# Kernel optimization log

Measured on AMD Instinct MI355X. Metric: run time of the kernel, lower is better.

## Reference

```python
import jax, jax.numpy as jnp
import numpy as np

LOAD = 0.001 / np.sqrt(2.0)  # diagonal loading applied to BOTH real and imag parts (faithful to source)


def setup_inputs() -> dict:
    key = jax.random.key(0)
    k1, k2, k3 = jax.random.split(key, 3)
    N, C, T, F = 8, 8, 600, 257
    mixture = jax.random.normal(k1, (N, 2, C, T, F), dtype=jnp.float32)
    noise = jax.random.normal(k2, (N, 2, C, T, F), dtype=jnp.float32)
    steering_vector = jax.random.normal(k3, (N, 2, F, C, 1), dtype=jnp.float32)
    return {"mixture": mixture, "noise": noise, "steering_vector": steering_vector}


def reference(mixture, noise, steering_vector):
    # to complex: RI dim is axis 1
    y = mixture[:, 0] + 1j * mixture[:, 1]            # [N,C,T,F]
    v = noise[:, 0] + 1j * noise[:, 1]                # [N,C,T,F]
    d = steering_vector[:, 0] + 1j * steering_vector[:, 1]  # [N,F,C,1]
    N, C, T, F = y.shape

    # time-averaged noise spatial covariance: mean_t v v^H  -> [N,F,C,C]
    phi = jnp.einsum('nctf,ndtf->nfcd', v, jnp.conj(v)) / T

    # diagonal loading: source adds load*eye to both real and imag stacks
    phi = phi + (LOAD + 1j * LOAD) * jnp.eye(C, dtype=phi.dtype)

    phi_inv = jnp.linalg.inv(phi)                     # [N,F,C,C]

    w_nume = phi_inv @ d                              # [N,F,C,1]
    dH = jnp.conj(jnp.swapaxes(d, -1, -2))            # [N,F,1,C]
    w_deno = dH @ phi_inv @ d                         # [N,F,1,1]
    w = w_nume / w_deno                               # [N,F,C,1]  (1x1 complex inverse)

    # beamform: X[n,t,f] = sum_c conj(w[n,f,c]) * y[n,c,t,f]
    X = jnp.einsum('nfc,nctf->ntf', jnp.conj(w[..., 0]), y)

    # back to RI-stacked [N,2,1,T,F]
    out = jnp.stack([X.real, X.imag], axis=1)[:, :, None]
    return out
```

## Files before the change

### kernel.cpp

```cpp
#include <hip/hip_runtime.h>

#define NN 8
#define CC 8
#define TT 600
#define FF 257
#define NF 2056
#define LOADING 7.0710678118654746e-04f

__global__ __launch_bounds__(256) void cov3_kernel(const float* __restrict__ noise,
                                                   float* __restrict__ partial,
                                                   int tc) {
    __shared__ float red[64][128];
    int lane = threadIdx.x & 63;
    int wave = threadIdx.x >> 6;
    int j = blockIdx.x * 64 + lane;
    int jc = j < NF ? j : NF - 1;
    int n = jc / FF;
    int f = jc - n * FF;

    int cend = min((int)(blockIdx.y + 1) * tc, TT);
    int tsub = (tc + 3) >> 2;
    int t0 = blockIdx.y * tc + wave * tsub;
    int t1 = min(t0 + tsub, cend);

    const float* base = noise + (size_t)n * (2 * CC * TT * FF) + f;

    float acc[64];
#pragma unroll
    for (int k = 0; k < 64; ++k) acc[k] = 0.f;

#pragma unroll 2
    for (int t = t0; t < t1; ++t) {
        float vr[CC], vi[CC];
#pragma unroll
        for (int c = 0; c < CC; ++c) {
            vr[c] = __builtin_nontemporal_load(&base[(c * TT + t) * FF]);
            vi[c] = __builtin_nontemporal_load(&base[((CC + c) * TT + t) * FF]);
        }
        int p = 0;
#pragma unroll
        for (int c = 0; c < CC; ++c) {
            acc[c] += vr[c] * vr[c] + vi[c] * vi[c];
#pragma unroll
            for (int d2 = c + 1; d2 < CC; ++d2) {
                acc[8 + p] += vr[c] * vr[d2] + vi[c] * vi[d2];
                acc[36 + p] += vi[c] * vr[d2] - vr[c] * vi[d2];
                ++p;
            }
        }
    }

    if (wave >= 2) {
        int col = threadIdx.x - 128;
#pragma unroll
        for (int k = 0; k < 64; ++k) red[k][col] = acc[k];
    }
    __syncthreads();
    if (wave < 2) {
#pragma unroll
        for (int k = 0; k < 64; ++k) acc[k] += red[k][threadIdx.x];
    }
    __syncthreads();
    if (wave == 1) {
#pragma unroll
        for (int k = 0; k < 64; ++k) red[k][lane] = acc[k];
    }
    __syncthreads();
    if (wave == 0 && j < NF) {
#pragma unroll
        for (int k = 0; k < 64; ++k) acc[k] += red[k][lane];
        float4* o = (float4*)(partial + ((size_t)blockIdx.y * NF + j) * 64);
#pragma unroll
        for (int k = 0; k < 16; ++k)
            o[k] = make_float4(acc[4 * k], acc[4 * k + 1], acc[4 * k + 2], acc[4 * k + 3]);
    }
}

__global__ __launch_bounds__(256) void solve2_kernel(const float* __restrict__ partial,
                                                     const float* __restrict__ steer,
                                                     float* __restrict__ wc,
                                                     int ntc) {
    __shared__ float sphi[4][64];
    int k = threadIdx.x & 63;
    int jj = threadIdx.x >> 6;
    int j = blockIdx.x * 4 + jj;

    float s = 0.f;
    for (int c = 0; c < ntc; ++c) s += partial[((size_t)c * NF + j) * 64 + k];
    sphi[jj][k] = s;
    __syncthreads();

    if (k != 0) return;
    int n = j / FF;
    int f = j - n * FF;

    const float invT = 1.0f / (float)TT;
    float Ar[CC][CC], Ai[CC][CC];
    {
        int p = 0;
#pragma unroll
        for (int c = 0; c < CC; ++c) {
            Ar[c][c] = sphi[jj][c] * invT + LOADING;
            Ai[c][c] = LOADING;
#pragma unroll
            for (int d2 = c + 1; d2 < CC; ++d2) {
                float re = sphi[jj][8 + p] * invT, im = sphi[jj][36 + p] * invT;
                Ar[c][d2] = re;  Ai[c][d2] = im;
                Ar[d2][c] = re;  Ai[d2][c] = -im;
                ++p;
            }
        }
    }

    float dr[CC], di[CC], br[CC], bi[CC];
#pragma unroll
    for (int c = 0; c < CC; ++c) {
        dr[c] = steer[((n * 2 + 0) * FF + f) * CC + c];
        di[c] = steer[((n * 2 + 1) * FF + f) * CC + c];
        br[c] = dr[c];
        bi[c] = di[c];
    }

#pragma unroll
    for (int kk = 0; kk < CC; ++kk) {
        float ar = Ar[kk][kk], ai = Ai[kk][kk];
        float sc = 1.0f / (ar * ar + ai * ai);
        float rr = ar * sc, ri = -ai * sc;
#pragma unroll
        for (int c = kk + 1; c < CC; ++c) {
            float xr0 = Ar[kk][c], xi0 = Ai[kk][c];
            Ar[kk][c] = xr0 * rr - xi0 * ri;
            Ai[kk][c] = xr0 * ri + xi0 * rr;
        }
        {
            float xr0 = br[kk], xi0 = bi[kk];
            br[kk] = xr0 * rr - xi0 * ri;
            bi[kk] = xr0 * ri + xi0 * rr;
        }
#pragma unroll
        for (int i = kk + 1; i < CC; ++i) {
            float mr = Ar[i][kk], mi = Ai[i][kk];
#pragma unroll
            for (int c = kk + 1; c < CC; ++c) {
                float kr = Ar[kk][c], ki = Ai[kk][c];
                Ar[i][c] -= mr * kr - mi * ki;
                Ai[i][c] -= mr * ki + mi * kr;
            }
            float bkr = br[kk], bki = bi[kk];
            br[i] -= mr * bkr - mi * bki;
            bi[i] -= mr * bki + mi * bkr;
        }
    }

    float xr[CC], xi[CC];
#pragma unroll
    for (int kk = CC - 1; kk >= 0; --kk) {
        float sr = br[kk], si = bi[kk];
#pragma unroll
        for (int c = kk + 1; c < CC; ++c) {
            sr -= Ar[kk][c] * xr[c] - Ai[kk][c] * xi[c];
            si -= Ar[kk][c] * xi[c] + Ai[kk][c] * xr[c];
        }
        xr[kk] = sr;
        xi[kk] = si;
    }

    float der = 0.f, dei = 0.f;
#pragma unroll
    for (int c = 0; c < CC; ++c) {
        der += dr[c] * xr[c] + di[c] * xi[c];
        dei += dr[c] * xi[c] - di[c] * xr[c];
    }
    float sc2 = 1.0f / (der * der + dei * dei);
    float* o = wc + (size_t)j * 16;
#pragma unroll
    for (int c = 0; c < CC; ++c) {
        float qr = (xr[c] * der + xi[c] * dei) * sc2;
        float qi = (xi[c] * der - xr[c] * dei) * sc2;
        o[2 * c] = qr;
        o[2 * c + 1] = -qi;
    }
}

__global__ __launch_bounds__(256) void bf2_kernel(const float* __restrict__ mix,
                                                  const float* __restrict__ wc,
                                                  float* __restrict__ out) {
    const int T2 = TT / 2;
    const int perN = T2 * FF;
    int idx = blockIdx.x * 256 + threadIdx.x;
    if (idx >= NN * perN) return;
    int n = idx / perN;
    int rem = idx - n * perN;
    int t2 = rem / FF;
    int f = rem - t2 * FF;
    int t = 2 * t2;

    const float4* w4 = (const float4*)(wc + ((size_t)(n * FF + f)) * 16);
    float4 w0 = w4[0], w1 = w4[1], w2 = w4[2], w3 = w4[3];
    float wr[CC] = {w0.x, w0.z, w1.x, w1.z, w2.x, w2.z, w3.x, w3.z};
    float wi[CC] = {w0.y, w0.w, w1.y, w1.w, w2.y, w2.w, w3.y, w3.w};

    const float* base = mix + (size_t)n * (2 * CC * TT * FF) + t * FF + f;
    float Xr0 = 0.f, Xi0 = 0.f, Xr1 = 0.f, Xi1 = 0.f;
#pragma unroll
    for (int c = 0; c < CC; ++c) {
        const float* br = base + (size_t)c * TT * FF;
        const float* bi = base + (size_t)(CC + c) * TT * FF;
        float yr0 = __builtin_nontemporal_load(br);
        float yi0 = __builtin_nontemporal_load(bi);
        float yr1 = __builtin_nontemporal_load(br + FF);
        float yi1 = __builtin_nontemporal_load(bi + FF);
        Xr0 += wr[c] * yr0 - wi[c] * yi0;
        Xi0 += wr[c] * yi0 + wi[c] * yr0;
        Xr1 += wr[c] * yr1 - wi[c] * yi1;
        Xi1 += wr[c] * yi1 + wi[c] * yr1;
    }
    float* oR = out + ((size_t)(n * 2 + 0) * TT + t) * FF + f;
    float* oI = out + ((size_t)(n * 2 + 1) * TT + t) * FF + f;
    __builtin_nontemporal_store(Xr0, oR);
    __builtin_nontemporal_store(Xr1, oR + FF);
    __builtin_nontemporal_store(Xi0, oI);
    __builtin_nontemporal_store(Xi1, oI + FF);
}

extern "C" void kernel_launch(void* const* d_in, const int* in_sizes, int n_in,
                              void* d_out, int out_size, void* d_ws, size_t ws_size,
                              hipStream_t stream) {
    const float* mixture = (const float*)d_in[0];
    const float* noise = (const float*)d_in[1];
    const float* steer = (const float*)d_in[2];
    float* out = (float*)d_out;

    float* partial = (float*)d_ws;
    size_t per_chunk = (size_t)NF * 64 * sizeof(float);
    size_t wc_bytes = (size_t)NF * 16 * sizeof(float);
    int ntc = 25;
    while (ntc > 1 && per_chunk * (size_t)ntc + wc_bytes > ws_size) --ntc;
    int tc = (TT + ntc - 1) / ntc;
    float* wcp = partial + (size_t)ntc * NF * 64;

    dim3 gcov((NF + 63) / 64, ntc);
    cov3_kernel<<<gcov, 256, 0, stream>>>(noise, partial, tc);
    solve2_kernel<<<NF / 4, 256, 0, stream>>>(partial, steer, wcp, ntc);
    int total2 = NN * (TT / 2) * FF;
    bf2_kernel<<<(total2 + 255) / 256, 256, 0, stream>>>(mixture, wcp, out);
}
```

Measured before the change: 214.3 us.

## Parallelize per-bin complex solve across 8 lanes with shuffles; add cov occupancy hint

The 8x8 complex Gaussian elimination is spread across 8 lanes, each holding one matrix row, instead of one thread per system. Pivot rows and back-substitution values are broadcast with warp shuffles, and the final d^H x dot product is done with a butterfly reduction. This shortens the long serial per-thread chain and the register pressure in the solve kernel. The covariance kernel also gets a min-blocks-per-CU launch bound of 2, which may cap registers and cause spills of its 64 accumulators.

Result: faster. 200.3 us (-6.5%).

```diff
diff --git a/kernel.cpp b/kernel.cpp
--- a/kernel.cpp
+++ b/kernel.cpp
@@ -7,9 +7,9 @@
 #define NF 2056
 #define LOADING 7.0710678118654746e-04f
 
-__global__ __launch_bounds__(256) void cov3_kernel(const float* __restrict__ noise,
-                                                   float* __restrict__ partial,
-                                                   int tc) {
+__global__ __launch_bounds__(256, 2) void cov3_kernel(const float* __restrict__ noise,
+                                                      float* __restrict__ partial,
+                                                      int tc) {
     __shared__ float red[64][128];
     int lane = threadIdx.x & 63;
     int wave = threadIdx.x >> 6;
@@ -76,110 +76,105 @@
     }
 }
 
-__global__ __launch_bounds__(256) void solve2_kernel(const float* __restrict__ partial,
+__global__ __launch_bounds__(256) void solve3_kernel(const float* __restrict__ partial,
                                                      const float* __restrict__ steer,
                                                      float* __restrict__ wc,
                                                      int ntc) {
     __shared__ float sphi[4][64];
-    int k = threadIdx.x & 63;
-    int jj = threadIdx.x >> 6;
-    int j = blockIdx.x * 4 + jj;
-
-    float s = 0.f;
-    for (int c = 0; c < ntc; ++c) s += partial[((size_t)c * NF + j) * 64 + k];
-    sphi[jj][k] = s;
-    __syncthreads();
-
-    if (k != 0) return;
+    {
+        int k = threadIdx.x & 63;
+        int jj = threadIdx.x >> 6;
+        int jsys = blockIdx.x * 4 + jj;
+        float s = 0.f;
+        for (int c = 0; c < ntc; ++c) s += partial[((size_t)c * NF + jsys) * 64 + k];
+        sphi[jj][k] = s;
+    }
+    __syncthreads();
+    if (threadIdx.x >= 32) return;
+
+    int lane = threadIdx.x;
+    int sys = lane >> 3;
+    int i = lane & 7;
+    int base = sys << 3;
+    int j = blockIdx.x * 4 + sys;
     int n = j / FF;
     int f = j - n * FF;
 
     const float invT = 1.0f / (float)TT;
-    float Ar[CC][CC], Ai[CC][CC];
-    {
-        int p = 0;
-#pragma unroll
-        for (int c = 0; c < CC; ++c) {
-            Ar[c][c] = sphi[jj][c] * invT + LOADING;
-            Ai[c][c] = LOADING;
-#pragma unroll
-            for (int d2 = c + 1; d2 < CC; ++d2) {
-                float re = sphi[jj][8 + p] * invT, im = sphi[jj][36 + p] * invT;
-                Ar[c][d2] = re;  Ai[c][d2] = im;
-                Ar[d2][c] = re;  Ai[d2][c] = -im;
-                ++p;
+    float Ar[CC], Ai[CC];
+#pragma unroll
+    for (int c = 0; c < CC; ++c) {
+        if (c == i) {
+            Ar[c] = sphi[sys][c] * invT + LOADING;
+            Ai[c] = LOADING;
+        } else {
+            int lo = i < c ? i : c;
+            int hi = i < c ? c : i;
+            int p = lo * (15 - lo) / 2 + hi - lo - 1;
+            float re = sphi[sys][8 + p] * invT;
+            float im = sphi[sys][36 + p] * invT;
+            Ar[c] = re;
+            Ai[c] = (i > c) ? -im : im;
+        }
+    }
+    float dr = steer[((n * 2 + 0) * FF + f) * CC + i];
+    float di = steer[((n * 2 + 1) * FF + f) * CC + i];
+    float br = dr, bi = di;
+
+#pragma unroll
+    for (int kk = 0; kk < CC; ++kk) {
+        float prr = __shfl(Ar[kk], base + kk);
+        float pii = __shfl(Ai[kk], base + kk);
+        float sc = 1.0f / (prr * prr + pii * pii);
+        float rr = prr * sc, ri = -pii * sc;
+        float mr = Ar[kk], mi = Ai[kk];
+        bool piv = (i == kk), below = (i > kk);
+#pragma unroll
+        for (int c = kk + 1; c < CC; ++c) {
+            float qr = __shfl(Ar[c], base + kk);
+            float qi = __shfl(Ai[c], base + kk);
+            float sr = qr * rr - qi * ri;
+            float si = qr * ri + qi * rr;
+            if (piv) { Ar[c] = sr; Ai[c] = si; }
+            else if (below) {
+                Ar[c] -= mr * sr - mi * si;
+                Ai[c] -= mr * si + mi * sr;
             }
         }
-    }
-
-    float dr[CC], di[CC], br[CC], bi[CC];
-#pragma unroll
-    for (int c = 0; c < CC; ++c) {
-        dr[c] = steer[((n * 2 + 0) * FF + f) * CC + c];
-        di[c] = steer[((n * 2 + 1) * FF + f) * CC + c];
-        br[c] = dr[c];
-        bi[c] = di[c];
-    }
-
-#pragma unroll
-    for (int kk = 0; kk < CC; ++kk) {
-        float ar = Ar[kk][kk], ai = Ai[kk][kk];
-        float sc = 1.0f / (ar * ar + ai * ai);
-        float rr = ar * sc, ri = -ai * sc;
-#pragma unroll
-        for (int c = kk + 1; c < CC; ++c) {
-            float xr0 = Ar[kk][c], xi0 = Ai[kk][c];
-            Ar[kk][c] = xr0 * rr - xi0 * ri;
-            Ai[kk][c] = xr0 * ri + xi0 * rr;
-        }
-        {
-            float xr0 = br[kk], xi0 = bi[kk];
-            br[kk] = xr0 * rr - xi0 * ri;
-            bi[kk] = xr0 * ri + xi0 * rr;
-        }
-#pragma unroll
-        for (int i = kk + 1; i < CC; ++i) {
-            float mr = Ar[i][kk], mi = Ai[i][kk];
-#pragma unroll
-            for (int c = kk + 1; c < CC; ++c) {
-                float kr = Ar[kk][c], ki = Ai[kk][c];
-                Ar[i][c] -= mr * kr - mi * ki;
-                Ai[i][c] -= mr * ki + mi * kr;
-            }
-            float bkr = br[kk], bki = bi[kk];
-            br[i] -= mr * bkr - mi * bki;
-            bi[i] -= mr * bki + mi * bkr;
-        }
-    }
-
-    float xr[CC], xi[CC];
+        float qbr = __shfl(br, base + kk);
+        float qbi = __shfl(bi, base + kk);
+        float sbr = qbr * rr - qbi * ri;
+        float sbi = qbr * ri + qbi * rr;
+        if (piv) { br = sbr; bi = sbi; }
+        else if (below) {
+            br -= mr * sbr - mi * sbi;
+            bi -= mr * sbi + mi * sbr;
+        }
+    }
+
 #pragma unroll
     for (int kk = CC - 1; kk >= 0; --kk) {
-        float sr = br[kk], si = bi[kk];
-#pragma unroll
-        for (int c = kk + 1; c < CC; ++c) {
-            sr -= Ar[kk][c] * xr[c] - Ai[kk][c] * xi[c];
-            si -= Ar[kk][c] * xi[c] + Ai[kk][c] * xr[c];
-        }
-        xr[kk] = sr;
-        xi[kk] = si;
-    }
-
-    float der = 0.f, dei = 0.f;
-#pragma unroll
-    for (int c = 0; c < CC; ++c) {
-        der += dr[c] * xr[c] + di[c] * xi[c];
-        dei += dr[c] * xi[c] - di[c] * xr[c];
-    }
-    float sc2 = 1.0f / (der * der + dei * dei);
-    float* o = wc + (size_t)j * 16;
-#pragma unroll
-    for (int c = 0; c < CC; ++c) {
-        float qr = (xr[c] * der + xi[c] * dei) * sc2;
-        float qi = (xi[c] * der - xr[c] * dei) * sc2;
-        o[2 * c] = qr;
-        o[2 * c + 1] = -qi;
-    }
+        float xkr = __shfl(br, base + kk);
+        float xki = __shfl(bi, base + kk);
+        if (i < kk) {
+            br -= Ar[kk] * xkr - Ai[kk] * xki;
+            bi -= Ar[kk] * xki + Ai[kk] * xkr;
+        }
+    }
+
+    float tr = dr * br + di * bi;
+    float ti = dr * bi - di * br;
+#pragma unroll
+    for (int m = 1; m < 8; m <<= 1) {
+        tr += __shfl_xor(tr, m);
+        ti += __shfl_xor(ti, m);
+    }
+    float sc2 = 1.0f / (tr * tr + ti * ti);
+    float qr = (br * tr + bi * ti) * sc2;
+    float qi = (bi * tr - br * ti) * sc2;
+    float* o = wc + (size_t)j * 16 + 2 * i;
+    o[0] = qr;
+    o[1] = -qi;
 }
 
 __global__ __launch_bounds__(256) void bf2_kernel(const float* __restrict__ mix,
@@ -241,7 +236,7 @@
 
     dim3 gcov((NF + 63) / 64, ntc);
     cov3_kernel<<<gcov, 256, 0, stream>>>(noise, partial, tc);
-    solve2_kernel<<<NF / 4, 256, 0, stream>>>(partial, steer, wcp, ntc);
+    solve3_kernel<<<NF / 4, 256, 0, stream>>>(partial, steer, wcp, ntc);
     int total2 = NN * (TT / 2) * FF;
     bf2_kernel<<<(total2 + 255) / 256, 256, 0, stream>>>(mixture, wcp, out);
 }
```
